# Kernel optimization log

Measured on AMD Instinct MI355X. Metric: run time of the kernel, lower is better.

## Reference

```python
import jax, jax.numpy as jnp
import numpy as np

N_USER, N_ITEM, N_REL = 200000, 100000, 64
DIM = 64
S_UU = S_UI = S_IU = S_II = 8
BATCH = 65536
MAX_RATING = 5.0


def setup_inputs() -> dict:
    key = jax.random.key(0)
    ks = jax.random.split(key, 24)
    inp = {}
    # query batch
    inp['u'] = jax.random.randint(ks[0], (BATCH,), 0, N_USER)
    inp['v'] = jax.random.randint(ks[1], (BATCH,), 0, N_ITEM)
    # embedding tables (init std=0.8 as in the torch code)
    inp['usr_feat'] = 0.8 * jax.random.normal(ks[2], (N_USER, DIM), jnp.float32)
    inp['item_feat'] = 0.8 * jax.random.normal(ks[3], (N_ITEM, DIM), jnp.float32)
    inp['rel_feat'] = 0.8 * jax.random.normal(ks[4], (N_REL, DIM), jnp.float32)
    # precomputed sampled neighbor tables (built once in __init__ in the original)
    inp['neigh_uu'] = jax.random.randint(ks[5], (N_USER, S_UU), 0, N_USER)
    inp['neigh_uu_st'] = jax.random.uniform(ks[6], (N_USER, S_UU), jnp.float32)
    inp['neigh_ui'] = jax.random.randint(ks[7], (N_USER, S_UI), 0, N_ITEM)
    inp['neigh_ui_rat'] = MAX_RATING * jax.random.uniform(ks[8], (N_USER, S_UI), jnp.float32)
    inp['neigh_ui_vot'] = jax.random.uniform(ks[9], (N_USER, S_UI), jnp.float32)
    inp['neigh_ui_tim'] = jax.random.uniform(ks[10], (N_USER, S_UI), jnp.float32)
    inp['neigh_iu'] = jax.random.randint(ks[11], (N_ITEM, S_IU), 0, N_USER)
    inp['neigh_iu_rat'] = MAX_RATING * jax.random.uniform(ks[12], (N_ITEM, S_IU), jnp.float32)
    inp['neigh_iu_vot'] = jax.random.uniform(ks[13], (N_ITEM, S_IU), jnp.float32)
    inp['neigh_iu_tim'] = jax.random.uniform(ks[14], (N_ITEM, S_IU), jnp.float32)
    inp['neigh_ii'] = jax.random.randint(ks[15], (N_ITEM, S_II), 0, N_ITEM)
    inp['neigh_ir'] = jax.random.randint(ks[16], (N_ITEM, S_II), 0, N_REL)
    # aggregator transforms (one per side)
    sc = 1.0 / np.sqrt(DIM)
    inp['Wu'] = sc * jax.random.normal(ks[17], (DIM, DIM), jnp.float32)
    inp['bu'] = jnp.zeros((DIM,), jnp.float32)
    inp['Wv'] = sc * jax.random.normal(ks[18], (DIM, DIM), jnp.float32)
    inp['bv'] = jnp.zeros((DIM,), jnp.float32)
    return inp


def reference(u, v, usr_feat, item_feat, rel_feat,
              neigh_uu, neigh_uu_st, neigh_ui, neigh_ui_rat, neigh_ui_vot, neigh_ui_tim,
              neigh_iu, neigh_iu_rat, neigh_iu_vot, neigh_iu_tim, neigh_ii, neigh_ir,
              Wu, bu, Wv, bv):
    u_emb = usr_feat[u]                                   # [B, D]
    v_emb = item_feat[v]                                  # [B, D]

    # ---- user-side aggregation ----
    # social neighbors, weighted by softmax over social tie strength
    uu_nei = usr_feat[neigh_uu[u]]                        # [B, S, D]
    w_uu = jax.nn.softmax(neigh_uu_st[u], axis=-1)        # [B, S]
    agg_uu = jnp.einsum('bs,bsd->bd', w_uu, uu_nei)
    # interacted items, weighted by rating * vote * time recency
    ui_nei = item_feat[neigh_ui[u]]                       # [B, S, D]
    s_ui = neigh_ui_rat[u] * neigh_ui_vot[u] * neigh_ui_tim[u]
    w_ui = jax.nn.softmax(s_ui, axis=-1)
    agg_ui = jnp.einsum('bs,bsd->bd', w_ui, ui_nei)
    user_h = jax.nn.relu((u_emb + agg_uu + agg_ui) @ Wu + bu)

    # ---- item-side aggregation ----
    # users who interacted with the item, weighted like above
    iu_nei = usr_feat[neigh_iu[v]]                        # [B, S, D]
    s_iu = neigh_iu_rat[v] * neigh_iu_vot[v] * neigh_iu_tim[v]
    w_iu = jax.nn.softmax(s_iu, axis=-1)
    agg_iu = jnp.einsum('bs,bsd->bd', w_iu, iu_nei)
    # KG neighbors with user-relation attention (KGCN-style)
    ii_nei = item_feat[neigh_ii[v]]                       # [B, S, D]
    rel = rel_feat[neigh_ir[v]]                           # [B, S, D]
    att = jnp.einsum('bd,bsd->bs', u_emb, rel)            # user-relation score
    w_ii = jax.nn.softmax(att, axis=-1)
    agg_ii = jnp.einsum('bs,bsd->bd', w_ii, ii_nei)
    item_h = jax.nn.relu((v_emb + agg_iu + agg_ii) @ Wv + bv)

    # rating prediction
    score = jax.nn.sigmoid(jnp.sum(user_h * item_h, axis=-1)) * MAX_RATING
    return score
```

## Files before the change

kernel.cpp:

```cpp
#include <hip/hip_runtime.h>
#include <math.h>

constexpr int DIM = 64;
constexpr int S = 8;
constexpr int WPB = 16;
constexpr int BLOCK = WPB * 64;
constexpr int GRID = 512;

typedef __attribute__((ext_vector_type(8))) __bf16 bf16x8;
typedef __attribute__((ext_vector_type(4))) float  f32x4;

#define LDS_FENCE() asm volatile("s_waitcnt lgkmcnt(0)" ::: "memory")

template <int CTRL>
__device__ __forceinline__ float dppx(float x) {
    return __builtin_bit_cast(float,
        __builtin_amdgcn_mov_dpp(__builtin_bit_cast(int, x), CTRL, 0xf, 0xf, true));
}
#define XOR1 0xB1
#define XOR2 0x4E

__device__ __forceinline__ unsigned pk_bf16(float a, float b) {
    unsigned ua = __builtin_bit_cast(unsigned, a);
    unsigned ub = __builtin_bit_cast(unsigned, b);
    ua = (ua + 0x8000u) >> 16;
    ub = (ub + 0x8000u) & 0xffff0000u;
    return ua | ub;
}

__device__ __forceinline__ void octet_softmax(float sc, float* wout) {
    float m = sc;
    m = fmaxf(m, dppx<XOR1>(m));
    m = fmaxf(m, dppx<XOR2>(m));
    m = fmaxf(m, __shfl_xor(m, 4));
    float e = __expf(sc - m);
    float s = e;
    s += dppx<XOR1>(s);
    s += dppx<XOR2>(s);
    s += __shfl_xor(s, 4);
    float w = e / s;
    #pragma unroll
    for (int k = 0; k < 8; k++) wout[k] = __shfl(w, k);
}

__device__ __forceinline__ void matvec_h(
    float xv, int lane, unsigned short* xw,
    const bf16x8* xa00, const bf16x8* xa01,
    const bf16x8* xa10, const bf16x8* xa11,
    const unsigned* bf,
    float b0, float b1, float b2, float b3,
    float& h0, float& h1, float& h2, float& h3)
{
    LDS_FENCE();
    const unsigned xb = __builtin_bit_cast(unsigned, xv);
    const unsigned hb = (xb + 0x8000u) & 0xffff0000u;
    const float xl = xv - __builtin_bit_cast(float, hb);
    xw[lane]      = (unsigned short)(hb >> 16);
    xw[64 + lane] = (unsigned short)((__builtin_bit_cast(unsigned, xl) + 0x8000u) >> 16);
    LDS_FENCE();

    f32x4 a0 = {0.f, 0.f, 0.f, 0.f};
    f32x4 a1 = a0, a2 = a0, a3 = a0;

    {
        const bf16x8 ah = *xa00, al = *xa01;
        const bf16x8 w0 = *(const bf16x8*)(bf);
        const bf16x8 w1 = *(const bf16x8*)(bf + 256);
        const bf16x8 w2 = *(const bf16x8*)(bf + 512);
        const bf16x8 w3 = *(const bf16x8*)(bf + 768);
        a0 = __builtin_amdgcn_mfma_f32_16x16x32_bf16(ah, w0, a0, 0, 0, 0);
        a0 = __builtin_amdgcn_mfma_f32_16x16x32_bf16(al, w0, a0, 0, 0, 0);
        a1 = __builtin_amdgcn_mfma_f32_16x16x32_bf16(ah, w1, a1, 0, 0, 0);
        a1 = __builtin_amdgcn_mfma_f32_16x16x32_bf16(al, w1, a1, 0, 0, 0);
        a2 = __builtin_amdgcn_mfma_f32_16x16x32_bf16(ah, w2, a2, 0, 0, 0);
        a2 = __builtin_amdgcn_mfma_f32_16x16x32_bf16(al, w2, a2, 0, 0, 0);
        a3 = __builtin_amdgcn_mfma_f32_16x16x32_bf16(ah, w3, a3, 0, 0, 0);
        a3 = __builtin_amdgcn_mfma_f32_16x16x32_bf16(al, w3, a3, 0, 0, 0);
    }
    {
        const bf16x8 ah = *xa10, al = *xa11;
        const bf16x8 w0 = *(const bf16x8*)(bf + 1024);
        const bf16x8 w1 = *(const bf16x8*)(bf + 1280);
        const bf16x8 w2 = *(const bf16x8*)(bf + 1536);
        const bf16x8 w3 = *(const bf16x8*)(bf + 1792);
        a0 = __builtin_amdgcn_mfma_f32_16x16x32_bf16(ah, w0, a0, 0, 0, 0);
        a0 = __builtin_amdgcn_mfma_f32_16x16x32_bf16(al, w0, a0, 0, 0, 0);
        a1 = __builtin_amdgcn_mfma_f32_16x16x32_bf16(ah, w1, a1, 0, 0, 0);
        a1 = __builtin_amdgcn_mfma_f32_16x16x32_bf16(al, w1, a1, 0, 0, 0);
        a2 = __builtin_amdgcn_mfma_f32_16x16x32_bf16(ah, w2, a2, 0, 0, 0);
        a2 = __builtin_amdgcn_mfma_f32_16x16x32_bf16(al, w2, a2, 0, 0, 0);
        a3 = __builtin_amdgcn_mfma_f32_16x16x32_bf16(ah, w3, a3, 0, 0, 0);
        a3 = __builtin_amdgcn_mfma_f32_16x16x32_bf16(al, w3, a3, 0, 0, 0);
    }

    h0 = fmaxf(a0[0] + b0, 0.f);
    h1 = fmaxf(a1[0] + b1, 0.f);
    h2 = fmaxf(a2[0] + b2, 0.f);
    h3 = fmaxf(a3[0] + b3, 0.f);
}

__global__ __launch_bounds__(BLOCK, 4)
void sestkgcn_kernel(
    const int*   __restrict__ u_idx,
    const int*   __restrict__ v_idx,
    const float* __restrict__ usr_feat,
    const float* __restrict__ item_feat,
    const float* __restrict__ rel_feat,
    const int*   __restrict__ neigh_uu,
    const float* __restrict__ neigh_uu_st,
    const int*   __restrict__ neigh_ui,
    const float* __restrict__ neigh_ui_rat,
    const float* __restrict__ neigh_ui_vot,
    const float* __restrict__ neigh_ui_tim,
    const int*   __restrict__ neigh_iu,
    const float* __restrict__ neigh_iu_rat,
    const float* __restrict__ neigh_iu_vot,
    const float* __restrict__ neigh_iu_tim,
    const int*   __restrict__ neigh_ii,
    const int*   __restrict__ neigh_ir,
    const float* __restrict__ Wu,
    const float* __restrict__ bu,
    const float* __restrict__ Wv,
    const float* __restrict__ bv,
    float*       __restrict__ out,
    int n)
{
    __shared__ unsigned sBFu[2048];
    __shared__ unsigned sBFv[2048];
    __shared__ __align__(16) unsigned short sX[WPB][128];

    const int tid = threadIdx.x;
    for (int i = tid; i < 2048; i += BLOCK) {
        const int d = i & 3, l = (i >> 2) & 63, f = i >> 8;
        const int row = ((f >> 2) << 5) + ((l >> 4) << 3) + (d << 1);
        const int col = ((f & 3) << 4) + (l & 15);
        sBFu[i] = pk_bf16(Wu[row * DIM + col], Wu[(row + 1) * DIM + col]);
        sBFv[i] = pk_bf16(Wv[row * DIM + col], Wv[(row + 1) * DIM + col]);
    }
    __syncthreads();

    const int wave = tid >> 6;
    const int lane = tid & 63;
    const int ls   = lane & 7;
    const int g    = lane >> 4;
    const int c    = lane & 15;

    unsigned short* xw = &sX[wave][0];
    const bf16x8* xa00 = (const bf16x8*)&sX[wave][g * 8];
    const bf16x8* xa01 = (const bf16x8*)&sX[wave][64 + g * 8];
    const bf16x8* xa10 = (const bf16x8*)&sX[wave][32 + g * 8];
    const bf16x8* xa11 = (const bf16x8*)&sX[wave][96 + g * 8];
    const unsigned* bfu = &sBFu[lane * 4];
    const unsigned* bfv = &sBFv[lane * 4];

    const float bu0 = bu[c], bu1 = bu[c + 16], bu2 = bu[c + 32], bu3 = bu[c + 48];
    const float bv0 = bv[c], bv1 = bv[c + 16], bv2 = bv[c + 32], bv3 = bv[c + 48];

    const int stride = GRID * WPB;
    int b = blockIdx.x * WPB + wave;
    if (b >= n) return;

    int u = u_idx[b];
    int v = v_idx[b];

    while (b < n) {
        const int b2 = b + stride;
        const int bc = (b2 < n) ? b2 : b;
        const int u_nxt = u_idx[bc];
        const int v_nxt = v_idx[bc];

        const unsigned u8 = (unsigned)u << 3, v8 = (unsigned)v << 3;

        const float u_d = usr_feat[((unsigned)u << 6) | (unsigned)lane];
        const float v_d = item_feat[((unsigned)v << 6) | (unsigned)lane];

        const float sc_uu = neigh_uu_st[u8 + ls];
        const float sc_ui = neigh_ui_rat[u8 + ls] * neigh_ui_vot[u8 + ls] * neigh_ui_tim[u8 + ls];
        const float sc_iu = neigh_iu_rat[v8 + ls] * neigh_iu_vot[v8 + ls] * neigh_iu_tim[v8 + ls];

        float w[S];
        octet_softmax(sc_uu, w);
        float agg_uu = 0.f;
        {
            const int4 i0 = ((const int4*)(neigh_uu + u8))[0];
            const int4 i1 = ((const int4*)(neigh_uu + u8))[1];
            const int ni[S] = {i0.x, i0.y, i0.z, i0.w, i1.x, i1.y, i1.z, i1.w};
            float r[S];
            #pragma unroll
            for (int s = 0; s < S; s++) r[s] = usr_feat[((unsigned)ni[s] << 6) | (unsigned)lane];
            #pragma unroll
            for (int s = 0; s < S; s++) agg_uu = fmaf(w[s], r[s], agg_uu);
        }

        octet_softmax(sc_ui, w);
        float agg_ui = 0.f;
        {
            const int4 i0 = ((const int4*)(neigh_ui + u8))[0];
            const int4 i1 = ((const int4*)(neigh_ui + u8))[1];
            const int ni[S] = {i0.x, i0.y, i0.z, i0.w, i1.x, i1.y, i1.z, i1.w};
            float r[S];
            #pragma unroll
            for (int s = 0; s < S; s++) r[s] = item_feat[((unsigned)ni[s] << 6) | (unsigned)lane];
            #pragma unroll
            for (int s = 0; s < S; s++) agg_ui = fmaf(w[s], r[s], agg_ui);
        }

        float hu0, hu1, hu2, hu3;
        matvec_h(u_d + agg_uu + agg_ui, lane, xw, xa00, xa01, xa10, xa11,
                 bfu, bu0, bu1, bu2, bu3, hu0, hu1, hu2, hu3);

        octet_softmax(sc_iu, w);
        float agg_iu = 0.f;
        {
            const int4 i0 = ((const int4*)(neigh_iu + v8))[0];
            const int4 i1 = ((const int4*)(neigh_iu + v8))[1];
            const int ni[S] = {i0.x, i0.y, i0.z, i0.w, i1.x, i1.y, i1.z, i1.w};
            float r[S];
            #pragma unroll
            for (int s = 0; s < S; s++) r[s] = usr_feat[((unsigned)ni[s] << 6) | (unsigned)lane];
            #pragma unroll
            for (int s = 0; s < S; s++) agg_iu = fmaf(w[s], r[s], agg_iu);
        }

        {
            const int4 r0 = ((const int4*)(neigh_ir + v8))[0];
            const int4 r1 = ((const int4*)(neigh_ir + v8))[1];
            const int nr[S] = {r0.x, r0.y, r0.z, r0.w, r1.x, r1.y, r1.z, r1.w};
            float p[S];
            #pragma unroll
            for (int s = 0; s < S; s++) p[s] = u_d * rel_feat[((unsigned)nr[s] << 6) | (unsigned)lane];

            float m1[4];
            #pragma unroll
            for (int i = 0; i < 4; i++) {
                float lo = (lane & 1) ? p[2 * i + 1] : p[2 * i];
                float hi = (lane & 1) ? p[2 * i]     : p[2 * i + 1];
                m1[i] = lo + dppx<XOR1>(hi);
            }
            float m2[2];
            #pragma unroll
            for (int i = 0; i < 2; i++) {
                float lo = (lane & 2) ? m1[2 * i + 1] : m1[2 * i];
                float hi = (lane & 2) ? m1[2 * i]     : m1[2 * i + 1];
                m2[i] = lo + dppx<XOR2>(hi);
            }
            float lo = (lane & 4) ? m2[1] : m2[0];
            float hi = (lane & 4) ? m2[0] : m2[1];
            float att = lo + __shfl_xor(hi, 4);
            att += __shfl_xor(att, 8);
            att += __shfl_xor(att, 16);
            att += __shfl_xor(att, 32);
            octet_softmax(att, w);
        }
        float agg_ii = 0.f;
        {
            const int4 i0 = ((const int4*)(neigh_ii + v8))[0];
            const int4 i1 = ((const int4*)(neigh_ii + v8))[1];
            const int ni[S] = {i0.x, i0.y, i0.z, i0.w, i1.x, i1.y, i1.z, i1.w};
            float r[S];
            #pragma unroll
            for (int s = 0; s < S; s++) r[s] = item_feat[((unsigned)ni[s] << 6) | (unsigned)lane];
            #pragma unroll
            for (int s = 0; s < S; s++) agg_ii = fmaf(w[s], r[s], agg_ii);
        }

        float hv0, hv1, hv2, hv3;
        matvec_h(v_d + agg_iu + agg_ii, lane, xw, xa00, xa01, xa10, xa11,
                 bfv, bv0, bv1, bv2, bv3, hv0, hv1, hv2, hv3);

        float p = hu0 * hv0 + hu1 * hv1 + hu2 * hv2 + hu3 * hv3;
        p += dppx<XOR1>(p);
        p += dppx<XOR2>(p);
        p += __shfl_xor(p, 4);
        p += __shfl_xor(p, 8);
        if (lane == 0) out[b] = 5.0f / (1.0f + __expf(-p));

        b = b2;
        u = u_nxt;
        v = v_nxt;
    }
}

extern "C" void kernel_launch(void* const* d_in, const int* in_sizes, int n_in,
                              void* d_out, int out_size, void* d_ws, size_t ws_size,
                              hipStream_t stream) {
    const int*   u_idx        = (const int*)  d_in[0];
    const int*   v_idx        = (const int*)  d_in[1];
    const float* usr_feat     = (const float*)d_in[2];
    const float* item_feat    = (const float*)d_in[3];
    const float* rel_feat     = (const float*)d_in[4];
    const int*   neigh_uu     = (const int*)  d_in[5];
    const float* neigh_uu_st  = (const float*)d_in[6];
    const int*   neigh_ui     = (const int*)  d_in[7];
    const float* neigh_ui_rat = (const float*)d_in[8];
    const float* neigh_ui_vot = (const float*)d_in[9];
    const float* neigh_ui_tim = (const float*)d_in[10];
    const int*   neigh_iu     = (const int*)  d_in[11];
    const float* neigh_iu_rat = (const float*)d_in[12];
    const float* neigh_iu_vot = (const float*)d_in[13];
    const float* neigh_iu_tim = (const float*)d_in[14];
    const int*   neigh_ii     = (const int*)  d_in[15];
    const int*   neigh_ir     = (const int*)  d_in[16];
    const float* Wu           = (const float*)d_in[17];
    const float* bu           = (const float*)d_in[18];
    const float* Wv           = (const float*)d_in[19];
    const float* bv           = (const float*)d_in[20];
    float*       out          = (float*)d_out;

    const int n = in_sizes[0];
    int blocks = (n + WPB - 1) / WPB;
    if (blocks > GRID) blocks = GRID;
    sestkgcn_kernel<<<blocks, BLOCK, 0, stream>>>(
        u_idx, v_idx, usr_feat, item_feat, rel_feat,
        neigh_uu, neigh_uu_st, neigh_ui, neigh_ui_rat, neigh_ui_vot, neigh_ui_tim,
        neigh_iu, neigh_iu_rat, neigh_iu_vot, neigh_iu_tim, neigh_ii, neigh_ir,
        Wu, bu, Wv, bv, out, n);
}
```

Before: 248.0 us.

## Hoist all neighbor gathers up front and shrink blocks to four waves

All five neighbor index loads and all 40 embedding-row gathers for a query are now issued together before any softmax or matvec work, so one long burst of memory latency replaces several serialized ones. Block size drops from 16 to 4 waves and grid doubles to 1024, so fewer waves share each block's LDS weight staging and more blocks are resident. The price is higher register pressure from holding 40 gathered values live, which may lower occupancy. Each block also still repacks the full weight matrices into LDS, now with fewer threads, and this happens more often overall.

Result: no change. 250.3 us (+0.9%).

```diff
diff --git a/kernel.cpp b/kernel.cpp
--- a/kernel.cpp
+++ b/kernel.cpp
@@ -3,9 +3,9 @@
 
 constexpr int DIM = 64;
 constexpr int S = 8;
-constexpr int WPB = 16;
+constexpr int WPB = 4;
 constexpr int BLOCK = WPB * 64;
-constexpr int GRID = 512;
+constexpr int GRID = 1024;
 
 typedef __attribute__((ext_vector_type(8))) __bf16 bf16x8;
 typedef __attribute__((ext_vector_type(4))) float  f32x4;
@@ -130,6 +130,7 @@
     __shared__ __align__(16) unsigned short sX[WPB][128];
 
     const int tid = threadIdx.x;
+    #pragma unroll
     for (int i = tid; i < 2048; i += BLOCK) {
         const int d = i & 3, l = (i >> 2) & 63, f = i >> 8;
         const int row = ((f >> 2) << 5) + ((l >> 4) << 3) + (d << 1);
@@ -178,32 +179,46 @@
         const float sc_ui = neigh_ui_rat[u8 + ls] * neigh_ui_vot[u8 + ls] * neigh_ui_tim[u8 + ls];
         const float sc_iu = neigh_iu_rat[v8 + ls] * neigh_iu_vot[v8 + ls] * neigh_iu_tim[v8 + ls];
 
+        const int4 iuu0 = ((const int4*)(neigh_uu + u8))[0];
+        const int4 iuu1 = ((const int4*)(neigh_uu + u8))[1];
+        const int4 iui0 = ((const int4*)(neigh_ui + u8))[0];
+        const int4 iui1 = ((const int4*)(neigh_ui + u8))[1];
+        const int4 iiu0 = ((const int4*)(neigh_iu + v8))[0];
+        const int4 iiu1 = ((const int4*)(neigh_iu + v8))[1];
+        const int4 iii0 = ((const int4*)(neigh_ii + v8))[0];
+        const int4 iii1 = ((const int4*)(neigh_ii + v8))[1];
+        const int4 iir0 = ((const int4*)(neigh_ir + v8))[0];
+        const int4 iir1 = ((const int4*)(neigh_ir + v8))[1];
+
+        float r_uu[S], r_ui[S], r_iu[S], r_ii[S], r_rel[S];
+        {
+            const int nuu[S] = {iuu0.x, iuu0.y, iuu0.z, iuu0.w, iuu1.x, iuu1.y, iuu1.z, iuu1.w};
+            const int nui[S] = {iui0.x, iui0.y, iui0.z, iui0.w, iui1.x, iui1.y, iui1.z, iui1.w};
+            const int niu[S] = {iiu0.x, iiu0.y, iiu0.z, iiu0.w, iiu1.x, iiu1.y, iiu1.z, iiu1.w};
+            const int nii[S] = {iii0.x, iii0.y, iii0.z, iii0.w, iii1.x, iii1.y, iii1.z, iii1.w};
+            const int nir[S] = {iir0.x, iir0.y, iir0.z, iir0.w, iir1.x, iir1.y, iir1.z, iir1.w};
+            #pragma unroll
+            for (int s = 0; s < S; s++) r_uu[s]  = usr_feat[((unsigned)nuu[s] << 6) | (unsigned)lane];
+            #pragma unroll
+            for (int s = 0; s < S; s++) r_ui[s]  = item_feat[((unsigned)nui[s] << 6) | (unsigned)lane];
+            #pragma unroll
+            for (int s = 0; s < S; s++) r_iu[s]  = usr_feat[((unsigned)niu[s] << 6) | (unsigned)lane];
+            #pragma unroll
+            for (int s = 0; s < S; s++) r_ii[s]  = item_feat[((unsigned)nii[s] << 6) | (unsigned)lane];
+            #pragma unroll
+            for (int s = 0; s < S; s++) r_rel[s] = rel_feat[((unsigned)nir[s] << 6) | (unsigned)lane];
+        }
+
         float w[S];
         octet_softmax(sc_uu, w);
         float agg_uu = 0.f;
-        {
-            const int4 i0 = ((const int4*)(neigh_uu + u8))[0];
-            const int4 i1 = ((const int4*)(neigh_uu + u8))[1];
-            const int ni[S] = {i0.x, i0.y, i0.z, i0.w, i1.x, i1.y, i1.z, i1.w};
-            float r[S];
-            #pragma unroll
-            for (int s = 0; s < S; s++) r[s] = usr_feat[((unsigned)ni[s] << 6) | (unsigned)lane];
-            #pragma unroll
-            for (int s = 0; s < S; s++) agg_uu = fmaf(w[s], r[s], agg_uu);
-        }
+        #pragma unroll
+        for (int s = 0; s < S; s++) agg_uu = fmaf(w[s], r_uu[s], agg_uu);
 
         octet_softmax(sc_ui, w);
         float agg_ui = 0.f;
-        {
-            const int4 i0 = ((const int4*)(neigh_ui + u8))[0];
-            const int4 i1 = ((const int4*)(neigh_ui + u8))[1];
-            const int ni[S] = {i0.x, i0.y, i0.z, i0.w, i1.x, i1.y, i1.z, i1.w};
-            float r[S];
-            #pragma unroll
-            for (int s = 0; s < S; s++) r[s] = item_feat[((unsigned)ni[s] << 6) | (unsigned)lane];
-            #pragma unroll
-            for (int s = 0; s < S; s++) agg_ui = fmaf(w[s], r[s], agg_ui);
-        }
+        #pragma unroll
+        for (int s = 0; s < S; s++) agg_ui = fmaf(w[s], r_ui[s], agg_ui);
 
         float hu0, hu1, hu2, hu3;
         matvec_h(u_d + agg_uu + agg_ui, lane, xw, xa00, xa01, xa10, xa11,
@@ -211,24 +226,13 @@
 
         octet_softmax(sc_iu, w);
         float agg_iu = 0.f;
+        #pragma unroll
+        for (int s = 0; s < S; s++) agg_iu = fmaf(w[s], r_iu[s], agg_iu);
+
         {
-            const int4 i0 = ((const int4*)(neigh_iu + v8))[0];
-            const int4 i1 = ((const int4*)(neigh_iu + v8))[1];
-            const int ni[S] = {i0.x, i0.y, i0.z, i0.w, i1.x, i1.y, i1.z, i1.w};
-            float r[S];
-            #pragma unroll
-            for (int s = 0; s < S; s++) r[s] = usr_feat[((unsigned)ni[s] << 6) | (unsigned)lane];
-            #pragma unroll
-            for (int s = 0; s < S; s++) agg_iu = fmaf(w[s], r[s], agg_iu);
-        }
-
-        {
-            const int4 r0 = ((const int4*)(neigh_ir + v8))[0];
-            const int4 r1 = ((const int4*)(neigh_ir + v8))[1];
-            const int nr[S] = {r0.x, r0.y, r0.z, r0.w, r1.x, r1.y, r1.z, r1.w};
             float p[S];
             #pragma unroll
-            for (int s = 0; s < S; s++) p[s] = u_d * rel_feat[((unsigned)nr[s] << 6) | (unsigned)lane];
+            for (int s = 0; s < S; s++) p[s] = u_d * r_rel[s];
 
             float m1[4];
             #pragma unroll
@@ -253,16 +257,8 @@
             octet_softmax(att, w);
         }
         float agg_ii = 0.f;
-        {
-            const int4 i0 = ((const int4*)(neigh_ii + v8))[0];
-            const int4 i1 = ((const int4*)(neigh_ii + v8))[1];
-            const int ni[S] = {i0.x, i0.y, i0.z, i0.w, i1.x, i1.y, i1.z, i1.w};
-            float r[S];
-            #pragma unroll
-            for (int s = 0; s < S; s++) r[s] = item_feat[((unsigned)ni[s] << 6) | (unsigned)lane];
-            #pragma unroll
-            for (int s = 0; s < S; s++) agg_ii = fmaf(w[s], r[s], agg_ii);
-        }
+        #pragma unroll
+        for (int s = 0; s < S; s++) agg_ii = fmaf(w[s], r_ii[s], agg_ii);
 
         float hv0, hv1, hv2, hv3;
         matvec_h(v_d + agg_iu + agg_ii, lane, xw, xa00, xa01, xa10, xa11,
```

## Batch 16 queries per block into one MFMA tile instead of per-query matvec

Applied to the files above, without the earlier changes.

Each of four waves now gathers and aggregates four queries and writes their bf16 hi/lo split inputs into shared, swizzled tiles. After a block barrier, each wave runs MFMA over all 16 queries for a 16-column slice of Wu and Wv, replacing a mostly wasted 16x16 MFMA per query. Partial dot products are reduced across waves through shared memory. This cuts MFMA and LDS work per query, but adds two block-wide barriers per 16 queries and changes block size and grid shape, which may reduce how many gathers are in flight.

Result: no change. 251.8 us (+1.5%).

```diff
diff --git a/kernel.cpp b/kernel.cpp
--- a/kernel.cpp
+++ b/kernel.cpp
@@ -3,14 +3,13 @@
 
 constexpr int DIM = 64;
 constexpr int S = 8;
-constexpr int WPB = 16;
+constexpr int WPB = 4;
 constexpr int BLOCK = WPB * 64;
-constexpr int GRID = 512;
+constexpr int QPB = 16;
+constexpr int GRID = 1024;
 
 typedef __attribute__((ext_vector_type(8))) __bf16 bf16x8;
 typedef __attribute__((ext_vector_type(4))) float  f32x4;
-
-#define LDS_FENCE() asm volatile("s_waitcnt lgkmcnt(0)" ::: "memory")
 
 template <int CTRL>
 __device__ __forceinline__ float dppx(float x) {
@@ -41,62 +40,6 @@
     float w = e / s;
     #pragma unroll
     for (int k = 0; k < 8; k++) wout[k] = __shfl(w, k);
-}
-
-__device__ __forceinline__ void matvec_h(
-    float xv, int lane, unsigned short* xw,
-    const bf16x8* xa00, const bf16x8* xa01,
-    const bf16x8* xa10, const bf16x8* xa11,
-    const unsigned* bf,
-    float b0, float b1, float b2, float b3,
-    float& h0, float& h1, float& h2, float& h3)
-{
-    LDS_FENCE();
-    const unsigned xb = __builtin_bit_cast(unsigned, xv);
-    const unsigned hb = (xb + 0x8000u) & 0xffff0000u;
-    const float xl = xv - __builtin_bit_cast(float, hb);
-    xw[lane]      = (unsigned short)(hb >> 16);
-    xw[64 + lane] = (unsigned short)((__builtin_bit_cast(unsigned, xl) + 0x8000u) >> 16);
-    LDS_FENCE();
-
-    f32x4 a0 = {0.f, 0.f, 0.f, 0.f};
-    f32x4 a1 = a0, a2 = a0, a3 = a0;
-
-    {
-        const bf16x8 ah = *xa00, al = *xa01;
-        const bf16x8 w0 = *(const bf16x8*)(bf);
-        const bf16x8 w1 = *(const bf16x8*)(bf + 256);
-        const bf16x8 w2 = *(const bf16x8*)(bf + 512);
-        const bf16x8 w3 = *(const bf16x8*)(bf + 768);
-        a0 = __builtin_amdgcn_mfma_f32_16x16x32_bf16(ah, w0, a0, 0, 0, 0);
-        a0 = __builtin_amdgcn_mfma_f32_16x16x32_bf16(al, w0, a0, 0, 0, 0);
-        a1 = __builtin_amdgcn_mfma_f32_16x16x32_bf16(ah, w1, a1, 0, 0, 0);
-        a1 = __builtin_amdgcn_mfma_f32_16x16x32_bf16(al, w1, a1, 0, 0, 0);
-        a2 = __builtin_amdgcn_mfma_f32_16x16x32_bf16(ah, w2, a2, 0, 0, 0);
-        a2 = __builtin_amdgcn_mfma_f32_16x16x32_bf16(al, w2, a2, 0, 0, 0);
-        a3 = __builtin_amdgcn_mfma_f32_16x16x32_bf16(ah, w3, a3, 0, 0, 0);
-        a3 = __builtin_amdgcn_mfma_f32_16x16x32_bf16(al, w3, a3, 0, 0, 0);
-    }
-    {
-        const bf16x8 ah = *xa10, al = *xa11;
-        const bf16x8 w0 = *(const bf16x8*)(bf + 1024);
-        const bf16x8 w1 = *(const bf16x8*)(bf + 1280);
-        const bf16x8 w2 = *(const bf16x8*)(bf + 1536);
-        const bf16x8 w3 = *(const bf16x8*)(bf + 1792);
-        a0 = __builtin_amdgcn_mfma_f32_16x16x32_bf16(ah, w0, a0, 0, 0, 0);
-        a0 = __builtin_amdgcn_mfma_f32_16x16x32_bf16(al, w0, a0, 0, 0, 0);
-        a1 = __builtin_amdgcn_mfma_f32_16x16x32_bf16(ah, w1, a1, 0, 0, 0);
-        a1 = __builtin_amdgcn_mfma_f32_16x16x32_bf16(al, w1, a1, 0, 0, 0);
-        a2 = __builtin_amdgcn_mfma_f32_16x16x32_bf16(ah, w2, a2, 0, 0, 0);
-        a2 = __builtin_amdgcn_mfma_f32_16x16x32_bf16(al, w2, a2, 0, 0, 0);
-        a3 = __builtin_amdgcn_mfma_f32_16x16x32_bf16(ah, w3, a3, 0, 0, 0);
-        a3 = __builtin_amdgcn_mfma_f32_16x16x32_bf16(al, w3, a3, 0, 0, 0);
-    }
-
-    h0 = fmaxf(a0[0] + b0, 0.f);
-    h1 = fmaxf(a1[0] + b1, 0.f);
-    h2 = fmaxf(a2[0] + b2, 0.f);
-    h3 = fmaxf(a3[0] + b3, 0.f);
 }
 
 __global__ __launch_bounds__(BLOCK, 4)
@@ -127,7 +70,11 @@
 {
     __shared__ unsigned sBFu[2048];
     __shared__ unsigned sBFv[2048];
-    __shared__ __align__(16) unsigned short sX[WPB][128];
+    __shared__ __align__(16) unsigned short sXuh[QPB * 64];
+    __shared__ __align__(16) unsigned short sXul[QPB * 64];
+    __shared__ __align__(16) unsigned short sXvh[QPB * 64];
+    __shared__ __align__(16) unsigned short sXvl[QPB * 64];
+    __shared__ __align__(16) float sP[WPB][QPB];
 
     const int tid = threadIdx.x;
     for (int i = tid; i < 2048; i += BLOCK) {
@@ -142,142 +89,203 @@
     const int wave = tid >> 6;
     const int lane = tid & 63;
     const int ls   = lane & 7;
-    const int g    = lane >> 4;
-    const int c    = lane & 15;
-
-    unsigned short* xw = &sX[wave][0];
-    const bf16x8* xa00 = (const bf16x8*)&sX[wave][g * 8];
-    const bf16x8* xa01 = (const bf16x8*)&sX[wave][64 + g * 8];
-    const bf16x8* xa10 = (const bf16x8*)&sX[wave][32 + g * 8];
-    const bf16x8* xa11 = (const bf16x8*)&sX[wave][96 + g * 8];
-    const unsigned* bfu = &sBFu[lane * 4];
-    const unsigned* bfv = &sBFv[lane * 4];
-
-    const float bu0 = bu[c], bu1 = bu[c + 16], bu2 = bu[c + 32], bu3 = bu[c + 48];
-    const float bv0 = bv[c], bv1 = bv[c + 16], bv2 = bv[c + 32], bv3 = bv[c + 48];
-
-    const int stride = GRID * WPB;
-    int b = blockIdx.x * WPB + wave;
-    if (b >= n) return;
-
-    int u = u_idx[b];
-    int v = v_idx[b];
-
-    while (b < n) {
-        const int b2 = b + stride;
-        const int bc = (b2 < n) ? b2 : b;
-        const int u_nxt = u_idx[bc];
-        const int v_nxt = v_idx[bc];
-
-        const unsigned u8 = (unsigned)u << 3, v8 = (unsigned)v << 3;
-
-        const float u_d = usr_feat[((unsigned)u << 6) | (unsigned)lane];
-        const float v_d = item_feat[((unsigned)v << 6) | (unsigned)lane];
-
-        const float sc_uu = neigh_uu_st[u8 + ls];
-        const float sc_ui = neigh_ui_rat[u8 + ls] * neigh_ui_vot[u8 + ls] * neigh_ui_tim[u8 + ls];
-        const float sc_iu = neigh_iu_rat[v8 + ls] * neigh_iu_vot[v8 + ls] * neigh_iu_tim[v8 + ls];
-
-        float w[S];
-        octet_softmax(sc_uu, w);
-        float agg_uu = 0.f;
+
+    const int qa = lane & 15;
+    const int ga = lane >> 4;
+    const int asz = (qa & 7) << 3;
+    const int a0 = qa * 64 + ((ga * 8) ^ asz);
+    const int a1 = qa * 64 + (((32 + ga * 8)) ^ asz);
+    const unsigned* bfu0 = &sBFu[(0 + wave) * 256 + lane * 4];
+    const unsigned* bfu1 = &sBFu[(4 + wave) * 256 + lane * 4];
+    const unsigned* bfv0 = &sBFv[(0 + wave) * 256 + lane * 4];
+    const unsigned* bfv1 = &sBFv[(4 + wave) * 256 + lane * 4];
+    const float bu_w = bu[wave * 16 + qa];
+    const float bv_w = bv[wave * 16 + qa];
+
+    const int bstep = GRID * QPB;
+    int b_base = blockIdx.x * QPB;
+    int b = b_base + 4 * wave;
+    int u, v;
+    {
+        const int bc = (b < n) ? b : (n - 1);
+        u = u_idx[bc];
+        v = v_idx[bc];
+    }
+
+    while (b_base < n) {
+        #pragma unroll 1
+        for (int j = 0; j < 4; j++) {
+            const int b_next = (j < 3) ? (b + 1) : (b_base + bstep + 4 * wave);
+            const int bnc = (b_next < n) ? b_next : (n - 1);
+            const int u_nxt = u_idx[bnc];
+            const int v_nxt = v_idx[bnc];
+
+            const unsigned u8 = (unsigned)u << 3, v8 = (unsigned)v << 3;
+
+            const float u_d = usr_feat[((unsigned)u << 6) | (unsigned)lane];
+            const float v_d = item_feat[((unsigned)v << 6) | (unsigned)lane];
+
+            const float sc_uu = neigh_uu_st[u8 + ls];
+            const float sc_ui = neigh_ui_rat[u8 + ls] * neigh_ui_vot[u8 + ls] * neigh_ui_tim[u8 + ls];
+            const float sc_iu = neigh_iu_rat[v8 + ls] * neigh_iu_vot[v8 + ls] * neigh_iu_tim[v8 + ls];
+
+            float w[S];
+            octet_softmax(sc_uu, w);
+            float agg_uu = 0.f;
+            {
+                const int4 i0 = ((const int4*)(neigh_uu + u8))[0];
+                const int4 i1 = ((const int4*)(neigh_uu + u8))[1];
+                const int ni[S] = {i0.x, i0.y, i0.z, i0.w, i1.x, i1.y, i1.z, i1.w};
+                float r[S];
+                #pragma unroll
+                for (int s = 0; s < S; s++) r[s] = usr_feat[((unsigned)ni[s] << 6) | (unsigned)lane];
+                #pragma unroll
+                for (int s = 0; s < S; s++) agg_uu = fmaf(w[s], r[s], agg_uu);
+            }
+
+            octet_softmax(sc_ui, w);
+            float agg_ui = 0.f;
+            {
+                const int4 i0 = ((const int4*)(neigh_ui + u8))[0];
+                const int4 i1 = ((const int4*)(neigh_ui + u8))[1];
+                const int ni[S] = {i0.x, i0.y, i0.z, i0.w, i1.x, i1.y, i1.z, i1.w};
+                float r[S];
+                #pragma unroll
+                for (int s = 0; s < S; s++) r[s] = item_feat[((unsigned)ni[s] << 6) | (unsigned)lane];
+                #pragma unroll
+                for (int s = 0; s < S; s++) agg_ui = fmaf(w[s], r[s], agg_ui);
+            }
+
+            octet_softmax(sc_iu, w);
+            float agg_iu = 0.f;
+            {
+                const int4 i0 = ((const int4*)(neigh_iu + v8))[0];
+                const int4 i1 = ((const int4*)(neigh_iu + v8))[1];
+                const int ni[S] = {i0.x, i0.y, i0.z, i0.w, i1.x, i1.y, i1.z, i1.w};
+                float r[S];
+                #pragma unroll
+                for (int s = 0; s < S; s++) r[s] = usr_feat[((unsigned)ni[s] << 6) | (unsigned)lane];
+                #pragma unroll
+                for (int s = 0; s < S; s++) agg_iu = fmaf(w[s], r[s], agg_iu);
+            }
+
+            {
+                const int4 r0 = ((const int4*)(neigh_ir + v8))[0];
+                const int4 r1 = ((const int4*)(neigh_ir + v8))[1];
+                const int nr[S] = {r0.x, r0.y, r0.z, r0.w, r1.x, r1.y, r1.z, r1.w};
+                float p[S];
+                #pragma unroll
+                for (int s = 0; s < S; s++) p[s] = u_d * rel_feat[((unsigned)nr[s] << 6) | (unsigned)lane];
+
+                float m1[4];
+                #pragma unroll
+                for (int i = 0; i < 4; i++) {
+                    float lo = (lane & 1) ? p[2 * i + 1] : p[2 * i];
+                    float hi = (lane & 1) ? p[2 * i]     : p[2 * i + 1];
+                    m1[i] = lo + dppx<XOR1>(hi);
+                }
+                float m2[2];
+                #pragma unroll
+                for (int i = 0; i < 2; i++) {
+                    float lo = (lane & 2) ? m1[2 * i + 1] : m1[2 * i];
+                    float hi = (lane & 2) ? m1[2 * i]     : m1[2 * i + 1];
+                    m2[i] = lo + dppx<XOR2>(hi);
+                }
+                float lo = (lane & 4) ? m2[1] : m2[0];
+                float hi = (lane & 4) ? m2[0] : m2[1];
+                float att = lo + __shfl_xor(hi, 4);
+                att += __shfl_xor(att, 8);
+                att += __shfl_xor(att, 16);
+                att += __shfl_xor(att, 32);
+                octet_softmax(att, w);
+            }
+            float agg_ii = 0.f;
+            {
+                const int4 i0 = ((const int4*)(neigh_ii + v8))[0];
+                const int4 i1 = ((const int4*)(neigh_ii + v8))[1];
+                const int ni[S] = {i0.x, i0.y, i0.z, i0.w, i1.x, i1.y, i1.z, i1.w};
+                float r[S];
+                #pragma unroll
+                for (int s = 0; s < S; s++) r[s] = item_feat[((unsigned)ni[s] << 6) | (unsigned)lane];
+                #pragma unroll
+                for (int s = 0; s < S; s++) agg_ii = fmaf(w[s], r[s], agg_ii);
+            }
+
+            const float xu = u_d + agg_uu + agg_ui;
+            const float xv = v_d + agg_iu + agg_ii;
+            const int ql = 4 * wave + j;
+            const int widx = ql * 64 + (lane ^ ((ql & 7) << 3));
+            {
+                const unsigned xb = __builtin_bit_cast(unsigned, xu);
+                const unsigned hb = (xb + 0x8000u) & 0xffff0000u;
+                const float xl = xu - __builtin_bit_cast(float, hb);
+                sXuh[widx] = (unsigned short)(hb >> 16);
+                sXul[widx] = (unsigned short)((__builtin_bit_cast(unsigned, xl) + 0x8000u) >> 16);
+            }
+            {
+                const unsigned xb = __builtin_bit_cast(unsigned, xv);
+                const unsigned hb = (xb + 0x8000u) & 0xffff0000u;
+                const float xl = xv - __builtin_bit_cast(float, hb);
+                sXvh[widx] = (unsigned short)(hb >> 16);
+                sXvl[widx] = (unsigned short)((__builtin_bit_cast(unsigned, xl) + 0x8000u) >> 16);
+            }
+
+            b = b_next;
+            u = u_nxt;
+            v = v_nxt;
+        }
+        __syncthreads();
+
         {
-            const int4 i0 = ((const int4*)(neigh_uu + u8))[0];
-            const int4 i1 = ((const int4*)(neigh_uu + u8))[1];
-            const int ni[S] = {i0.x, i0.y, i0.z, i0.w, i1.x, i1.y, i1.z, i1.w};
-            float r[S];
+            const bf16x8 Auh0 = *(const bf16x8*)&sXuh[a0];
+            const bf16x8 Aul0 = *(const bf16x8*)&sXul[a0];
+            const bf16x8 Auh1 = *(const bf16x8*)&sXuh[a1];
+            const bf16x8 Aul1 = *(const bf16x8*)&sXul[a1];
+            const bf16x8 Avh0 = *(const bf16x8*)&sXvh[a0];
+            const bf16x8 Avl0 = *(const bf16x8*)&sXvl[a0];
+            const bf16x8 Avh1 = *(const bf16x8*)&sXvh[a1];
+            const bf16x8 Avl1 = *(const bf16x8*)&sXvl[a1];
+            const bf16x8 Bu0 = *(const bf16x8*)bfu0;
+            const bf16x8 Bu1 = *(const bf16x8*)bfu1;
+            const bf16x8 Bv0 = *(const bf16x8*)bfv0;
+            const bf16x8 Bv1 = *(const bf16x8*)bfv1;
+
+            f32x4 au = {0.f, 0.f, 0.f, 0.f};
+            f32x4 av = {0.f, 0.f, 0.f, 0.f};
+            au = __builtin_amdgcn_mfma_f32_16x16x32_bf16(Auh0, Bu0, au, 0, 0, 0);
+            au = __builtin_amdgcn_mfma_f32_16x16x32_bf16(Aul0, Bu0, au, 0, 0, 0);
+            au = __builtin_amdgcn_mfma_f32_16x16x32_bf16(Auh1, Bu1, au, 0, 0, 0);
+            au = __builtin_amdgcn_mfma_f32_16x16x32_bf16(Aul1, Bu1, au, 0, 0, 0);
+            av = __builtin_amdgcn_mfma_f32_16x16x32_bf16(Avh0, Bv0, av, 0, 0, 0);
+            av = __builtin_amdgcn_mfma_f32_16x16x32_bf16(Avl0, Bv0, av, 0, 0, 0);
+            av = __builtin_amdgcn_mfma_f32_16x16x32_bf16(Avh1, Bv1, av, 0, 0, 0);
+            av = __builtin_amdgcn_mfma_f32_16x16x32_bf16(Avl1, Bv1, av, 0, 0, 0);
+
+            float pr[4];
             #pragma unroll
-            for (int s = 0; s < S; s++) r[s] = usr_feat[((unsigned)ni[s] << 6) | (unsigned)lane];
-            #pragma unroll
-            for (int s = 0; s < S; s++) agg_uu = fmaf(w[s], r[s], agg_uu);
+            for (int r = 0; r < 4; r++) {
+                const float hu = fmaxf(au[r] + bu_w, 0.f);
+                const float hv = fmaxf(av[r] + bv_w, 0.f);
+                float p = hu * hv;
+                p += dppx<XOR1>(p);
+                p += dppx<XOR2>(p);
+                p += __shfl_xor(p, 4);
+                p += __shfl_xor(p, 8);
+                pr[r] = p;
+            }
+            if ((lane & 15) == 0) {
+                *(float4*)&sP[wave][ga * 4] = make_float4(pr[0], pr[1], pr[2], pr[3]);
+            }
         }
-
-        octet_softmax(sc_ui, w);
-        float agg_ui = 0.f;
-        {
-            const int4 i0 = ((const int4*)(neigh_ui + u8))[0];
-            const int4 i1 = ((const int4*)(neigh_ui + u8))[1];
-            const int ni[S] = {i0.x, i0.y, i0.z, i0.w, i1.x, i1.y, i1.z, i1.w};
-            float r[S];
-            #pragma unroll
-            for (int s = 0; s < S; s++) r[s] = item_feat[((unsigned)ni[s] << 6) | (unsigned)lane];
-            #pragma unroll
-            for (int s = 0; s < S; s++) agg_ui = fmaf(w[s], r[s], agg_ui);
+        __syncthreads();
+
+        if (tid < QPB) {
+            const float p = sP[0][tid] + sP[1][tid] + sP[2][tid] + sP[3][tid];
+            const int bq = b_base + tid;
+            if (bq < n) out[bq] = 5.0f / (1.0f + __expf(-p));
         }
 
-        float hu0, hu1, hu2, hu3;
-        matvec_h(u_d + agg_uu + agg_ui, lane, xw, xa00, xa01, xa10, xa11,
-                 bfu, bu0, bu1, bu2, bu3, hu0, hu1, hu2, hu3);
-
-        octet_softmax(sc_iu, w);
-        float agg_iu = 0.f;
-        {
-            const int4 i0 = ((const int4*)(neigh_iu + v8))[0];
-            const int4 i1 = ((const int4*)(neigh_iu + v8))[1];
-            const int ni[S] = {i0.x, i0.y, i0.z, i0.w, i1.x, i1.y, i1.z, i1.w};
-            float r[S];
-            #pragma unroll
-            for (int s = 0; s < S; s++) r[s] = usr_feat[((unsigned)ni[s] << 6) | (unsigned)lane];
-            #pragma unroll
-            for (int s = 0; s < S; s++) agg_iu = fmaf(w[s], r[s], agg_iu);
-        }
-
-        {
-            const int4 r0 = ((const int4*)(neigh_ir + v8))[0];
-            const int4 r1 = ((const int4*)(neigh_ir + v8))[1];
-            const int nr[S] = {r0.x, r0.y, r0.z, r0.w, r1.x, r1.y, r1.z, r1.w};
-            float p[S];
-            #pragma unroll
-            for (int s = 0; s < S; s++) p[s] = u_d * rel_feat[((unsigned)nr[s] << 6) | (unsigned)lane];
-
-            float m1[4];
-            #pragma unroll
-            for (int i = 0; i < 4; i++) {
-                float lo = (lane & 1) ? p[2 * i + 1] : p[2 * i];
-                float hi = (lane & 1) ? p[2 * i]     : p[2 * i + 1];
-                m1[i] = lo + dppx<XOR1>(hi);
-            }
-            float m2[2];
-            #pragma unroll
-            for (int i = 0; i < 2; i++) {
-                float lo = (lane & 2) ? m1[2 * i + 1] : m1[2 * i];
-                float hi = (lane & 2) ? m1[2 * i]     : m1[2 * i + 1];
-                m2[i] = lo + dppx<XOR2>(hi);
-            }
-            float lo = (lane & 4) ? m2[1] : m2[0];
-            float hi = (lane & 4) ? m2[0] : m2[1];
-            float att = lo + __shfl_xor(hi, 4);
-            att += __shfl_xor(att, 8);
-            att += __shfl_xor(att, 16);
-            att += __shfl_xor(att, 32);
-            octet_softmax(att, w);
-        }
-        float agg_ii = 0.f;
-        {
-            const int4 i0 = ((const int4*)(neigh_ii + v8))[0];
-            const int4 i1 = ((const int4*)(neigh_ii + v8))[1];
-            const int ni[S] = {i0.x, i0.y, i0.z, i0.w, i1.x, i1.y, i1.z, i1.w};
-            float r[S];
-            #pragma unroll
-            for (int s = 0; s < S; s++) r[s] = item_feat[((unsigned)ni[s] << 6) | (unsigned)lane];
-            #pragma unroll
-            for (int s = 0; s < S; s++) agg_ii = fmaf(w[s], r[s], agg_ii);
-        }
-
-        float hv0, hv1, hv2, hv3;
-        matvec_h(v_d + agg_iu + agg_ii, lane, xw, xa00, xa01, xa10, xa11,
-                 bfv, bv0, bv1, bv2, bv3, hv0, hv1, hv2, hv3);
-
-        float p = hu0 * hv0 + hu1 * hv1 + hu2 * hv2 + hu3 * hv3;
-        p += dppx<XOR1>(p);
-        p += dppx<XOR2>(p);
-        p += __shfl_xor(p, 4);
-        p += __shfl_xor(p, 8);
-        if (lane == 0) out[b] = 5.0f / (1.0f + __expf(-p));
-
-        b = b2;
-        u = u_nxt;
-        v = v_nxt;
+        b_base += bstep;
     }
 }
 
@@ -308,7 +316,7 @@
     float*       out          = (float*)d_out;
 
     const int n = in_sizes[0];
-    int blocks = (n + WPB - 1) / WPB;
+    int blocks = (n + QPB - 1) / QPB;
     if (blocks > GRID) blocks = GRID;
     sestkgcn_kernel<<<blocks, BLOCK, 0, stream>>>(
         u_idx, v_idx, usr_feat, item_feat, rel_feat,
```

## Gather embedding rows from per-call fp16 copies of user and item tables

Applied to the files above, without the earlier changes.

Adds a conversion kernel that writes fp16 copies of the user and item embedding tables into the workspace on every call. The main kernel, templated on a flag, then gathers neighbour rows from these half-width tables, halving the bytes fetched per random row access. The aim is to cut gather traffic and raise cache hit rates, at the cost of a full-table conversion pass each call and reduced precision in the neighbour features. The launch-bounds occupancy hint is also dropped from the main kernel.

New measurement: 275.3 us. 1.11x slower.

```diff
diff --git a/kernel.cpp b/kernel.cpp
--- a/kernel.cpp
+++ b/kernel.cpp
@@ -7,8 +7,16 @@
 constexpr int BLOCK = WPB * 64;
 constexpr int GRID = 512;
 
+constexpr int N_USER = 200000;
+constexpr int N_ITEM = 100000;
+constexpr size_t USR16_BYTES  = (size_t)N_USER * DIM * 2;
+constexpr size_t ITEM16_BYTES = (size_t)N_ITEM * DIM * 2;
+constexpr size_t WS_NEEDED    = USR16_BYTES + ITEM16_BYTES;
+
 typedef __attribute__((ext_vector_type(8))) __bf16 bf16x8;
 typedef __attribute__((ext_vector_type(4))) float  f32x4;
+typedef __attribute__((ext_vector_type(8))) float     f32x8;
+typedef __attribute__((ext_vector_type(8))) _Float16  f16x8;
 
 #define LDS_FENCE() asm volatile("s_waitcnt lgkmcnt(0)" ::: "memory")
 
@@ -99,7 +107,22 @@
     h3 = fmaxf(a3[0] + b3, 0.f);
 }
 
-__global__ __launch_bounds__(BLOCK, 4)
+__global__ __launch_bounds__(256)
+void cvt16_kernel(const float* __restrict__ usr_feat, const float* __restrict__ item_feat,
+                  _Float16* __restrict__ usr16, _Float16* __restrict__ item16,
+                  int n8u, int n8t)
+{
+    const int i = blockIdx.x * 256 + threadIdx.x;
+    if (i >= n8t) return;
+    const float* src = (i < n8u) ? usr_feat : item_feat;
+    _Float16*   dst = (i < n8u) ? usr16    : item16;
+    const int j = (i < n8u) ? i : (i - n8u);
+    const f32x8 v = ((const f32x8*)src)[j];
+    ((f16x8*)dst)[j] = __builtin_convertvector(v, f16x8);
+}
+
+template <bool USE16>
+__global__ __launch_bounds__(BLOCK)
 void sestkgcn_kernel(
     const int*   __restrict__ u_idx,
     const int*   __restrict__ v_idx,
@@ -122,6 +145,8 @@
     const float* __restrict__ bu,
     const float* __restrict__ Wv,
     const float* __restrict__ bv,
+    const _Float16* __restrict__ usr16,
+    const _Float16* __restrict__ item16,
     float*       __restrict__ out,
     int n)
 {
@@ -187,7 +212,10 @@
             const int ni[S] = {i0.x, i0.y, i0.z, i0.w, i1.x, i1.y, i1.z, i1.w};
             float r[S];
             #pragma unroll
-            for (int s = 0; s < S; s++) r[s] = usr_feat[((unsigned)ni[s] << 6) | (unsigned)lane];
+            for (int s = 0; s < S; s++) {
+                const unsigned ix = ((unsigned)ni[s] << 6) | (unsigned)lane;
+                r[s] = USE16 ? (float)usr16[ix] : usr_feat[ix];
+            }
             #pragma unroll
             for (int s = 0; s < S; s++) agg_uu = fmaf(w[s], r[s], agg_uu);
         }
@@ -200,7 +228,10 @@
             const int ni[S] = {i0.x, i0.y, i0.z, i0.w, i1.x, i1.y, i1.z, i1.w};
             float r[S];
             #pragma unroll
-            for (int s = 0; s < S; s++) r[s] = item_feat[((unsigned)ni[s] << 6) | (unsigned)lane];
+            for (int s = 0; s < S; s++) {
+                const unsigned ix = ((unsigned)ni[s] << 6) | (unsigned)lane;
+                r[s] = USE16 ? (float)item16[ix] : item_feat[ix];
+            }
             #pragma unroll
             for (int s = 0; s < S; s++) agg_ui = fmaf(w[s], r[s], agg_ui);
         }
@@ -217,7 +248,10 @@
             const int ni[S] = {i0.x, i0.y, i0.z, i0.w, i1.x, i1.y, i1.z, i1.w};
             float r[S];
             #pragma unroll
-            for (int s = 0; s < S; s++) r[s] = usr_feat[((unsigned)ni[s] << 6) | (unsigned)lane];
+            for (int s = 0; s < S; s++) {
+                const unsigned ix = ((unsigned)ni[s] << 6) | (unsigned)lane;
+                r[s] = USE16 ? (float)usr16[ix] : usr_feat[ix];
+            }
             #pragma unroll
             for (int s = 0; s < S; s++) agg_iu = fmaf(w[s], r[s], agg_iu);
         }
@@ -259,7 +293,10 @@
             const int ni[S] = {i0.x, i0.y, i0.z, i0.w, i1.x, i1.y, i1.z, i1.w};
             float r[S];
             #pragma unroll
-            for (int s = 0; s < S; s++) r[s] = item_feat[((unsigned)ni[s] << 6) | (unsigned)lane];
+            for (int s = 0; s < S; s++) {
+                const unsigned ix = ((unsigned)ni[s] << 6) | (unsigned)lane;
+                r[s] = USE16 ? (float)item16[ix] : item_feat[ix];
+            }
             #pragma unroll
             for (int s = 0; s < S; s++) agg_ii = fmaf(w[s], r[s], agg_ii);
         }
@@ -310,9 +347,25 @@
     const int n = in_sizes[0];
     int blocks = (n + WPB - 1) / WPB;
     if (blocks > GRID) blocks = GRID;
-    sestkgcn_kernel<<<blocks, BLOCK, 0, stream>>>(
-        u_idx, v_idx, usr_feat, item_feat, rel_feat,
-        neigh_uu, neigh_uu_st, neigh_ui, neigh_ui_rat, neigh_ui_vot, neigh_ui_tim,
-        neigh_iu, neigh_iu_rat, neigh_iu_vot, neigh_iu_tim, neigh_ii, neigh_ir,
-        Wu, bu, Wv, bv, out, n);
-}
+
+    const bool use16 = (d_ws != nullptr) && (ws_size >= WS_NEEDED);
+    if (use16) {
+        _Float16* usr16  = (_Float16*)d_ws;
+        _Float16* item16 = (_Float16*)((char*)d_ws + USR16_BYTES);
+        const int n8u = N_USER * DIM / 8;
+        const int n8t = n8u + N_ITEM * DIM / 8;
+        cvt16_kernel<<<(n8t + 255) / 256, 256, 0, stream>>>(
+            usr_feat, item_feat, usr16, item16, n8u, n8t);
+        sestkgcn_kernel<true><<<blocks, BLOCK, 0, stream>>>(
+            u_idx, v_idx, usr_feat, item_feat, rel_feat,
+            neigh_uu, neigh_uu_st, neigh_ui, neigh_ui_rat, neigh_ui_vot, neigh_ui_tim,
+            neigh_iu, neigh_iu_rat, neigh_iu_vot, neigh_iu_tim, neigh_ii, neigh_ir,
+            Wu, bu, Wv, bv, usr16, item16, out, n);
+    } else {
+        sestkgcn_kernel<false><<<blocks, BLOCK, 0, stream>>>(
+            u_idx, v_idx, usr_feat, item_feat, rel_feat,
+            neigh_uu, neigh_uu_st, neigh_ui, neigh_ui_rat, neigh_ui_vot, neigh_ui_tim,
+            neigh_iu, neigh_iu_rat, neigh_iu_vot, neigh_iu_tim, neigh_ii, neigh_ir,
+            Wu, bu, Wv, bv, nullptr, nullptr, out, n);
+    }
+}
```
